# Optimization experiments

Measured on AMD Instinct MI355X. Metric: run time of the kernel, lower is better.

Reference implementation:

```python
import jax, jax.numpy as jnp
import numpy as np

BATCH, IN, HID, OUT = 8192, 784, 4096, 10


def setup_inputs() -> dict:
    key = jax.random.key(0)
    k_x, k_w1, k_b1, k_w2, k_b2 = jax.random.split(key, 5)
    return {
        "x": jax.random.normal(k_x, (BATCH, IN), dtype=jnp.float32),
        "W1": jax.random.normal(k_w1, (HID, IN), dtype=jnp.float32) * 0.05,
        "b1": jax.random.normal(k_b1, (HID,), dtype=jnp.float32) * 0.05,
        "W2": jax.random.normal(k_w2, (OUT, HID), dtype=jnp.float32) * 0.05,
        "b2": jax.random.normal(k_b2, (OUT,), dtype=jnp.float32) * 0.05,
    }


def reference(x, W1, b1, W2, b2):
    # x: [B, 784] -- first layer, so the input is NOT binarized (BNN convention
    # for in_features == 784); only the weight is sign-quantized.
    x = x.reshape(-1, IN)
    Wb1 = jnp.sign(W1)                       # binarized weights in {-1, 0, +1}
    h = jnp.einsum("bi,hi->bh", x, Wb1) + b1  # BinarizeLinear fc1
    h = jnp.clip(h, -1.0, 1.0)               # Hardtanh
    out = jnp.einsum("bh,oh->bo", h, W2) + b2  # plain float fc2
    return out
```

## Files before the change

kernel.cpp:

```cpp
#include <hip/hip_runtime.h>
#include <cstdint>


#define BATCH 8192
#define IN_F  784
#define HID   4096
#define OUT_F 10
#define KP    832
#define NKT   13
#define BM    256
#define BN    256
#define BK    64
#define NCT   (HID / BN)
#define HCS   264

typedef unsigned short u16;
typedef __attribute__((ext_vector_type(4))) unsigned short u16x4;
typedef __attribute__((ext_vector_type(8)))  _Float16 f16x8;
typedef __attribute__((ext_vector_type(4)))  float    f32x4;
typedef __attribute__((ext_vector_type(16))) float    f32x16;

#define BARRIER() do { asm volatile("" ::: "memory"); \
                       __builtin_amdgcn_s_barrier();  \
                       asm volatile("" ::: "memory"); } while (0)
#define WAITV(n)  asm volatile("s_waitcnt vmcnt(" #n ")" ::: "memory")
#define WAITL0()  asm volatile("s_waitcnt lgkmcnt(0)" ::: "memory")

__device__ __forceinline__ u16 f2h(float f) {
  union { _Float16 h; u16 u; } c;
  c.h = (_Float16)f;
  return c.u;
}

__device__ __forceinline__ void gl_lds16(const void* g, void* l) {
  __builtin_amdgcn_global_load_lds(
      (const __attribute__((address_space(1))) uint32_t*)g,
      (__attribute__((address_space(3))) uint32_t*)l, 16, 0, 0);
}

__global__ void prep_kernel(const float* __restrict__ x, const float* __restrict__ W1,
                            const float* __restrict__ W2,
                            u16* __restrict__ xh, u16* __restrict__ wh,
                            u16* __restrict__ w2h) {
  const int stride = gridDim.x * blockDim.x;
  const int gid = blockIdx.x * blockDim.x + threadIdx.x;
  const int KP4 = KP / 4;
  const int IN4 = IN_F / 4;
  const float4* x4 = (const float4*)x;
  const float4* w4 = (const float4*)W1;
  for (int i = gid; i < BATCH * KP4; i += stride) {
    int b = i / KP4, k = i - b * KP4;
    u16x4 o = {0, 0, 0, 0};
    if (k < IN4) {
      float4 v = x4[(size_t)b * IN4 + k];
      o[0] = f2h(v.x); o[1] = f2h(v.y); o[2] = f2h(v.z); o[3] = f2h(v.w);
    }
    *(u16x4*)&xh[(size_t)b * KP + k * 4] = o;
  }
  for (int i = gid; i < HID * KP4; i += stride) {
    int h = i / KP4, k = i - h * KP4;
    u16x4 o = {0, 0, 0, 0};
    if (k < IN4) {
      float4 v = w4[(size_t)h * IN4 + k];
      o[0] = v.x > 0.f ? 0x3C00 : (v.x < 0.f ? 0xBC00 : 0);
      o[1] = v.y > 0.f ? 0x3C00 : (v.y < 0.f ? 0xBC00 : 0);
      o[2] = v.z > 0.f ? 0x3C00 : (v.z < 0.f ? 0xBC00 : 0);
      o[3] = v.w > 0.f ? 0x3C00 : (v.w < 0.f ? 0xBC00 : 0);
    }
    *(u16x4*)&wh[(size_t)h * KP + k * 4] = o;
  }
  for (int i = gid; i < 16 * HID; i += stride) {
    int o = i >> 12, k = i & (HID - 1);
    w2h[i] = (o < OUT_F) ? f2h(W2[o * HID + k]) : (u16)0;
  }
}

__global__ void __launch_bounds__(512, 1) gemm_kernel(
    const u16* __restrict__ xh, const u16* __restrict__ wh,
    const u16* __restrict__ w2h, const float* __restrict__ b1,
    float* __restrict__ part) {
  __shared__ union {
    struct { u16 A[2][BM * BK]; u16 B[3][BN * BK]; } m;
    struct { u16 hc[128 * HCS]; u16 w2[16 * 256]; } e;
  } sm;

  const int t   = threadIdx.x;
  const int ct  = blockIdx.x;
  const int br  = blockIdx.y;
  const int w   = t >> 6;
  const int l   = t & 63;
  const int wm  = w >> 2;
  const int wn  = w & 3;
  const int lo  = l & 31;
  const int hi  = l >> 5;
  const int g   = l >> 4;
  const int r16 = l & 15;

  const int  srow  = t >> 3;
  const int  sslot = (t & 7) ^ (srow & 7);
  const u16* gA = xh + (size_t)(br * BM) * KP + sslot * 8;
  const u16* gB = wh + (size_t)(ct * BN) * KP + sslot * 8;

  auto stA2 = [&](int tile, int h) {
    const int b = tile & 1;
#pragma unroll
    for (int c = 2 * h; c < 2 * h + 2; ++c)
      gl_lds16(gA + (size_t)(c * 64 + srow) * KP + tile * BK,
               &sm.m.A[b][c * 4096 + t * 8]);
  };
  auto stB = [&](int tile, int s) {
#pragma unroll
    for (int c = 0; c < 4; ++c)
      gl_lds16(gB + (size_t)(c * 64 + srow) * KP + tile * BK,
               &sm.m.B[s][c * 4096 + t * 8]);
  };
  auto rdA = [&](int p, int mi, int kk) -> f16x8 {
    int row = mi * 64 + wm * 32 + lo;
    return *(const f16x8*)&sm.m.A[p][row * 64 + (((kk * 2 + hi) ^ (row & 7)) << 3)];
  };
  auto rdB = [&](int s, int nh, int kk) -> f16x8 {
    int row = nh * 128 + wn * 32 + lo;
    return *(const f16x8*)&sm.m.B[s][row * 64 + (((kk * 2 + hi) ^ (row & 7)) << 3)];
  };

  f32x16 acc[4][2] = {};

  stA2(0, 0); stA2(0, 1);
  stB(0, 0);
  stB(1, 1);
  WAITV(4);
  BARRIER();

  int bs = 0;
  for (int tt = 0; tt < NKT; ++tt) {
    const int  p      = tt & 1;
    const int  bs2    = (bs >= 1) ? bs - 1 : 2;
    const bool a_more = (tt + 1 < NKT);
    const bool b_more = (tt + 2 < NKT);
#pragma unroll
    for (int kk = 0; kk < 4; ++kk) {
      f16x8 af[4], bf[2];
#pragma unroll
      for (int mi = 0; mi < 4; ++mi) af[mi] = rdA(p, mi, kk);
#pragma unroll
      for (int nh = 0; nh < 2; ++nh) bf[nh] = rdB(bs, nh, kk);
      if      (kk == 0) { if (a_more) stA2(tt + 1, 0); }
      else if (kk == 1) { if (a_more) stA2(tt + 1, 1); }
      else if (kk == 2) { if (b_more) stB(tt + 2, bs2); }
      else              { if (tt < NKT - 2) WAITV(4); else WAITV(0); }
      BARRIER();
      WAITL0();
      __builtin_amdgcn_sched_barrier(0);
      __builtin_amdgcn_s_setprio(1);
#pragma unroll
      for (int mi = 0; mi < 4; ++mi)
#pragma unroll
        for (int nh = 0; nh < 2; ++nh)
          acc[mi][nh] = __builtin_amdgcn_mfma_f32_32x32x16_f16(
              af[mi], bf[nh], acc[mi][nh], 0, 0, 0);
      __builtin_amdgcn_s_setprio(0);
      BARRIER();
    }
    bs = (bs == 2) ? 0 : bs + 1;
  }

  {
    int row = t >> 5, sp = t & 31;
    int ls = (sp & 24) | ((sp ^ row) & 7);
    gl_lds16(w2h + (size_t)row * HID + ct * BN + ls * 8, &sm.e.w2[t * 8]);
  }
  float b1v[2];
#pragma unroll
  for (int nh = 0; nh < 2; ++nh) b1v[nh] = b1[ct * BN + nh * 128 + wn * 32 + lo];

  float* partBase = part + ((size_t)ct * BATCH + br * BM) * 16;

#pragma unroll
  for (int p = 0; p < 2; ++p) {
    if (p == 1) BARRIER();
#pragma unroll
    for (int mi = 0; mi < 2; ++mi)
#pragma unroll
      for (int nh = 0; nh < 2; ++nh)
#pragma unroll
        for (int r = 0; r < 16; ++r) {
          float v = acc[p * 2 + mi][nh][r] + b1v[nh];
          v = fminf(fmaxf(v, -1.f), 1.f);
          int crow = (r & 3) + 8 * (r >> 2) + 4 * hi;
          sm.e.hc[(mi * 64 + wm * 32 + crow) * HCS + nh * 128 + wn * 32 + lo] = f2h(v);
        }
    if (p == 0) { WAITV(0); }
    BARRIER();
    f32x4 acc2 = {};
#pragma unroll
    for (int kk = 0; kk < 8; ++kk) {
      f16x8 a2 = *(const f16x8*)&sm.e.hc[(w * 16 + r16) * HCS + kk * 32 + g * 8];
      int s   = kk * 4 + g;
      int sp2 = (s & 24) | ((s ^ r16) & 7);
      f16x8 b2f = *(const f16x8*)&sm.e.w2[r16 * 256 + sp2 * 8];
      acc2 = __builtin_amdgcn_mfma_f32_16x16x32_f16(a2, b2f, acc2, 0, 0, 0);
    }
#pragma unroll
    for (int r = 0; r < 4; ++r)
      partBase[(size_t)(p * 128 + w * 16 + g * 4 + r) * 16 + r16] = acc2[r];
  }
}

__global__ void reduce_kernel(const float* __restrict__ part, const float* __restrict__ b2,
                              float* __restrict__ out) {
  int i = blockIdx.x * blockDim.x + threadIdx.x;
  if (i >= BATCH * OUT_F) return;
  int b = i / OUT_F, o = i - b * OUT_F;
  float acc = b2[o];
#pragma unroll
  for (int c = 0; c < NCT; ++c)
    acc += part[((size_t)c * BATCH + b) * 16 + o];
  out[i] = acc;
}

extern "C" void kernel_launch(void* const* d_in, const int* in_sizes, int n_in,
                              void* d_out, int out_size, void* d_ws, size_t ws_size,
                              hipStream_t stream) {
  const float* x  = (const float*)d_in[0];
  const float* W1 = (const float*)d_in[1];
  const float* b1 = (const float*)d_in[2];
  const float* W2 = (const float*)d_in[3];
  const float* b2 = (const float*)d_in[4];
  float* out = (float*)d_out;

  u16* xh  = (u16*)d_ws;
  u16* wh  = xh + (size_t)BATCH * KP;
  u16* w2h = wh + (size_t)HID * KP;
  float* part = (float*)(w2h + 16 * HID);

  hipLaunchKernelGGL(prep_kernel, dim3(2048), dim3(256), 0, stream, x, W1, W2, xh, wh, w2h);
  hipLaunchKernelGGL(gemm_kernel, dim3(NCT, BATCH / BM), dim3(512), 0, stream,
                     xh, wh, w2h, b1, part);
  hipLaunchKernelGGL(reduce_kernel, dim3((BATCH * OUT_F + 255) / 256), dim3(256), 0, stream,
                     part, b2, out);
}
```

Measured before the change: 71.41 us.

## Switch main GEMM to 16x16x32 MFMA with per-wave 128x64 tiles and fewer barriers

Replaces the 32x32x16 MFMA tiling (4x2 tiles per wave) with 16x16x32 MFMA and an 8x4 grid of accumulators per wave, so each wave owns a contiguous 128x64 block. The K-loop now runs two half-tile steps per BK instead of four, issuing the whole A-tile prefetch at once and cutting the barriers per tile from eight to at most four. The epilogue is reorganized so only waves whose row half matches the current pass write hidden activations. The goal is less synchronization overhead and fewer LDS fragment loads per MFMA. In exchange, register pressure goes up with 8 A fragments and 4 B fragments live at once, and the grouped A prefetch could change how well loads overlap with compute.

```diff
diff --git a/kernel.cpp b/kernel.cpp
--- a/kernel.cpp
+++ b/kernel.cpp
@@ -18,7 +18,6 @@
 typedef __attribute__((ext_vector_type(4))) unsigned short u16x4;
 typedef __attribute__((ext_vector_type(8)))  _Float16 f16x8;
 typedef __attribute__((ext_vector_type(4)))  float    f32x4;
-typedef __attribute__((ext_vector_type(16))) float    f32x16;
 
 #define BARRIER() do { asm volatile("" ::: "memory"); \
                        __builtin_amdgcn_s_barrier();  \
@@ -91,20 +90,19 @@
   const int l   = t & 63;
   const int wm  = w >> 2;
   const int wn  = w & 3;
-  const int lo  = l & 31;
-  const int hi  = l >> 5;
   const int g   = l >> 4;
   const int r16 = l & 15;
+  const int swz = (r16 & 7) << 3;
 
   const int  srow  = t >> 3;
   const int  sslot = (t & 7) ^ (srow & 7);
   const u16* gA = xh + (size_t)(br * BM) * KP + sslot * 8;
   const u16* gB = wh + (size_t)(ct * BN) * KP + sslot * 8;
 
-  auto stA2 = [&](int tile, int h) {
+  auto stA = [&](int tile) {
     const int b = tile & 1;
 #pragma unroll
-    for (int c = 2 * h; c < 2 * h + 2; ++c)
+    for (int c = 0; c < 4; ++c)
       gl_lds16(gA + (size_t)(c * 64 + srow) * KP + tile * BK,
                &sm.m.A[b][c * 4096 + t * 8]);
   };
@@ -115,17 +113,17 @@
                &sm.m.B[s][c * 4096 + t * 8]);
   };
   auto rdA = [&](int p, int mi, int kk) -> f16x8 {
-    int row = mi * 64 + wm * 32 + lo;
-    return *(const f16x8*)&sm.m.A[p][row * 64 + (((kk * 2 + hi) ^ (row & 7)) << 3)];
-  };
-  auto rdB = [&](int s, int nh, int kk) -> f16x8 {
-    int row = nh * 128 + wn * 32 + lo;
-    return *(const f16x8*)&sm.m.B[s][row * 64 + (((kk * 2 + hi) ^ (row & 7)) << 3)];
-  };
-
-  f32x16 acc[4][2] = {};
-
-  stA2(0, 0); stA2(0, 1);
+    int row = wm * 128 + mi * 16 + r16;
+    return *(const f16x8*)&sm.m.A[p][row * 64 + ((kk * 32 + g * 8) ^ swz)];
+  };
+  auto rdB = [&](int s, int nj, int kk) -> f16x8 {
+    int row = wn * 64 + nj * 16 + r16;
+    return *(const f16x8*)&sm.m.B[s][row * 64 + ((kk * 32 + g * 8) ^ swz)];
+  };
+
+  f32x4 acc[8][4] = {};
+
+  stA(0);
   stB(0, 0);
   stB(1, 1);
   WAITV(4);
@@ -133,62 +131,77 @@
 
   int bs = 0;
   for (int tt = 0; tt < NKT; ++tt) {
-    const int  p      = tt & 1;
-    const int  bs2    = (bs >= 1) ? bs - 1 : 2;
-    const bool a_more = (tt + 1 < NKT);
-    const bool b_more = (tt + 2 < NKT);
-#pragma unroll
-    for (int kk = 0; kk < 4; ++kk) {
-      f16x8 af[4], bf[2];
-#pragma unroll
-      for (int mi = 0; mi < 4; ++mi) af[mi] = rdA(p, mi, kk);
-#pragma unroll
-      for (int nh = 0; nh < 2; ++nh) bf[nh] = rdB(bs, nh, kk);
-      if      (kk == 0) { if (a_more) stA2(tt + 1, 0); }
-      else if (kk == 1) { if (a_more) stA2(tt + 1, 1); }
-      else if (kk == 2) { if (b_more) stB(tt + 2, bs2); }
-      else              { if (tt < NKT - 2) WAITV(4); else WAITV(0); }
-      BARRIER();
-      WAITL0();
-      __builtin_amdgcn_sched_barrier(0);
-      __builtin_amdgcn_s_setprio(1);
-#pragma unroll
-      for (int mi = 0; mi < 4; ++mi)
-#pragma unroll
-        for (int nh = 0; nh < 2; ++nh)
-          acc[mi][nh] = __builtin_amdgcn_mfma_f32_32x32x16_f16(
-              af[mi], bf[nh], acc[mi][nh], 0, 0, 0);
-      __builtin_amdgcn_s_setprio(0);
-      BARRIER();
-    }
+    const int p   = tt & 1;
+    const int bs2 = (bs >= 1) ? bs - 1 : 2;
+    f16x8 af[8], bf[4];
+
+#pragma unroll
+    for (int mi = 0; mi < 8; ++mi) af[mi] = rdA(p, mi, 0);
+#pragma unroll
+    for (int nj = 0; nj < 4; ++nj) bf[nj] = rdB(bs, nj, 0);
+    if (tt + 1 < NKT) stA(tt + 1);
+    WAITL0();
+    __builtin_amdgcn_sched_barrier(0);
+    __builtin_amdgcn_s_setprio(1);
+#pragma unroll
+    for (int mi = 0; mi < 8; ++mi)
+#pragma unroll
+      for (int nj = 0; nj < 4; ++nj)
+        acc[mi][nj] = __builtin_amdgcn_mfma_f32_16x16x32_f16(
+            af[mi], bf[nj], acc[mi][nj], 0, 0, 0);
+    __builtin_amdgcn_s_setprio(0);
+
+#pragma unroll
+    for (int mi = 0; mi < 8; ++mi) af[mi] = rdA(p, mi, 1);
+#pragma unroll
+    for (int nj = 0; nj < 4; ++nj) bf[nj] = rdB(bs, nj, 1);
+    if (tt + 2 < NKT) stB(tt + 2, bs2);
+    if      (tt < NKT - 2)  { WAITV(4); }
+    else if (tt == NKT - 2) { WAITV(0); }
+    if (tt < NKT - 1) BARRIER();
+    WAITL0();
+    __builtin_amdgcn_sched_barrier(0);
+    __builtin_amdgcn_s_setprio(1);
+#pragma unroll
+    for (int mi = 0; mi < 8; ++mi)
+#pragma unroll
+      for (int nj = 0; nj < 4; ++nj)
+        acc[mi][nj] = __builtin_amdgcn_mfma_f32_16x16x32_f16(
+            af[mi], bf[nj], acc[mi][nj], 0, 0, 0);
+    __builtin_amdgcn_s_setprio(0);
+    if (tt < NKT - 1) BARRIER();
+
     bs = (bs == 2) ? 0 : bs + 1;
   }
 
+  WAITL0();
+  BARRIER();
   {
     int row = t >> 5, sp = t & 31;
     int ls = (sp & 24) | ((sp ^ row) & 7);
     gl_lds16(w2h + (size_t)row * HID + ct * BN + ls * 8, &sm.e.w2[t * 8]);
   }
-  float b1v[2];
-#pragma unroll
-  for (int nh = 0; nh < 2; ++nh) b1v[nh] = b1[ct * BN + nh * 128 + wn * 32 + lo];
+  float b1v[4];
+#pragma unroll
+  for (int ni = 0; ni < 4; ++ni) b1v[ni] = b1[ct * BN + wn * 64 + ni * 16 + r16];
 
   float* partBase = part + ((size_t)ct * BATCH + br * BM) * 16;
 
 #pragma unroll
   for (int p = 0; p < 2; ++p) {
     if (p == 1) BARRIER();
-#pragma unroll
-    for (int mi = 0; mi < 2; ++mi)
-#pragma unroll
-      for (int nh = 0; nh < 2; ++nh)
-#pragma unroll
-        for (int r = 0; r < 16; ++r) {
-          float v = acc[p * 2 + mi][nh][r] + b1v[nh];
-          v = fminf(fmaxf(v, -1.f), 1.f);
-          int crow = (r & 3) + 8 * (r >> 2) + 4 * hi;
-          sm.e.hc[(mi * 64 + wm * 32 + crow) * HCS + nh * 128 + wn * 32 + lo] = f2h(v);
-        }
+    if (wm == p) {
+#pragma unroll
+      for (int mi = 0; mi < 8; ++mi)
+#pragma unroll
+        for (int ni = 0; ni < 4; ++ni)
+#pragma unroll
+          for (int r = 0; r < 4; ++r) {
+            float v = acc[mi][ni][r] + b1v[ni];
+            v = fminf(fmaxf(v, -1.f), 1.f);
+            sm.e.hc[(mi * 16 + g * 4 + r) * HCS + wn * 64 + ni * 16 + r16] = f2h(v);
+          }
+    }
     if (p == 0) { WAITV(0); }
     BARRIER();
     f32x4 acc2 = {};
```

Result: faster. 64.00 us (-10.4%).
